# Kernel tuning notes

Hardware: AMD Instinct MI355X
Metric: run time of the kernel (lower is better)

The kernel has to match this reference:

```python
import jax, jax.numpy as jnp
import numpy as np

L = 3        # layer_num
D = 64       # hidden_size (input_dim)
NU = 100000  # user nodes in batched graph
NI = 100000  # item nodes in batched graph
NUSER = 200000  # user vocab
NITEM = 200000  # item vocab
E = 1000000  # edges per relation ('by' and 'pby')
B = 1024     # target users per batch


def _time_enc(t, freq, phase):
    # TimeEncode: cos(t * basis_freq + phase), per edge -> [E, D]
    return jnp.cos(t[:, None] * freq[None, :] + phase[None, :])


def _seg_attn(e, vals, dst, num_seg):
    # softmax of e over edges sharing a destination node, then weighted sum of vals
    m = jax.ops.segment_max(e, dst, num_segments=num_seg)
    ex = jnp.exp(e - m[dst])
    denom = jax.ops.segment_sum(ex, dst, num_segments=num_seg)
    alpha = ex / denom[dst]
    return jax.ops.segment_sum(alpha[:, None] * vals, dst, num_segments=num_seg)


def _forward(user_emb, item_emb, Wu, Wi, Wuu, Wii,
             u_freq, u_phase, uk_freq, uk_phase,
             i_freq, i_phase, ik_freq, ik_phase,
             unified_W, dense_W, dense_b,
             by_time, pby_time,
             user_id, item_id, by_src, by_dst, pby_src, pby_dst,
             user_index, last_item_index):
    nu = user_id.shape[0]
    ni = item_id.shape[0]
    d = user_emb.shape[1]
    scale = 1.0 / jnp.sqrt(jnp.float32(d))
    user_h = user_emb[user_id]   # [NU, D]
    item_h = item_emb[item_id]   # [NI, D]
    user_layers = []
    n_layers = Wu.shape[0]
    for l in range(n_layers):
        uh = user_h @ Wu[l]   # user_weight
        ih = item_h @ Wi[l]   # item_weight
        # --- 'by' relation: item -> user (user_reduce_func) ---
        src_i = ih[by_src]    # mailbox['item_h']
        dst_u = uh[by_dst]    # mailbox['user_h'] (dst feature)
        e_u = jnp.sum((_time_enc(by_time, u_freq[l], u_phase[l]) + src_i) * dst_u, -1) * scale
        agg_u = _seg_attn(e_u, src_i + _time_enc(by_time, uk_freq[l], uk_phase[l]), by_dst, nu)
        # --- 'pby' relation: user -> item (item_reduce_func) ---
        src_u = uh[pby_src]
        dst_i = ih[pby_dst]
        e_i = jnp.sum((_time_enc(pby_time, i_freq[l], i_phase[l]) + src_u) * dst_i, -1) * scale
        agg_i = _seg_attn(e_i, src_u + _time_enc(pby_time, ik_freq[l], ik_phase[l]), pby_dst, ni)
        # node update: elu(W [agg ; old])
        user_h = jax.nn.elu(jnp.concatenate([agg_u, user_h], -1) @ Wuu[l])
        item_h = jax.nn.elu(jnp.concatenate([agg_i, item_h], -1) @ Wii[l])
        user_layers.append(user_h[user_index])
    user_layers.append(item_h[last_item_index])  # last_item=True
    unified = jnp.concatenate(user_layers, -1) @ unified_W
    return jax.nn.relu(unified @ dense_W + dense_b)  # [B, 3]


def setup_inputs() -> dict:
    key = jax.random.key(0)
    ks = jax.random.split(key, 20)
    w = lambda k, shape: jax.random.normal(k, shape, jnp.float32) * 0.05
    freq0 = jnp.asarray(1.0 / 10 ** np.linspace(0, 9, D), dtype=jnp.float32)
    freq = jnp.tile(freq0[None], (L, 1))
    zph = jnp.zeros((L, D), jnp.float32)
    return {
        'user_emb': w(ks[0], (NUSER, D)),
        'item_emb': w(ks[1], (NITEM, D)),
        'Wu': w(ks[2], (L, D, D)),
        'Wi': w(ks[3], (L, D, D)),
        'Wuu': w(ks[4], (L, 2 * D, D)),
        'Wii': w(ks[5], (L, 2 * D, D)),
        'u_freq': freq, 'u_phase': zph,
        'uk_freq': freq, 'uk_phase': zph,
        'i_freq': freq, 'i_phase': zph,
        'ik_freq': freq, 'ik_phase': zph,
        'unified_W': w(ks[6], ((L + 1) * D, D)),
        'dense_W': w(ks[7], (D, 3)),
        'dense_b': jnp.zeros((3,), jnp.float32),
        'by_time': jax.random.uniform(ks[8], (E,), jnp.float32),
        'pby_time': jax.random.uniform(ks[9], (E,), jnp.float32),
        'user_id': jax.random.randint(ks[10], (NU,), 0, NUSER),
        'item_id': jax.random.randint(ks[11], (NI,), 0, NITEM),
        'by_src': jax.random.randint(ks[12], (E,), 0, NI),
        'by_dst': jax.random.randint(ks[13], (E,), 0, NU),
        'pby_src': jax.random.randint(ks[14], (E,), 0, NU),
        'pby_dst': jax.random.randint(ks[15], (E,), 0, NI),
        'user_index': jax.random.randint(ks[16], (B,), 0, NU),
        'last_item_index': jax.random.randint(ks[17], (B,), 0, NI),
    }


def reference(user_emb, item_emb, Wu, Wi, Wuu, Wii,
              u_freq, u_phase, uk_freq, uk_phase,
              i_freq, i_phase, ik_freq, ik_phase,
              unified_W, dense_W, dense_b,
              by_time, pby_time,
              user_id, item_id, by_src, by_dst, pby_src, pby_dst,
              user_index, last_item_index):
    return _forward(user_emb, item_emb, Wu, Wi, Wuu, Wii,
                    u_freq, u_phase, uk_freq, uk_phase,
                    i_freq, i_phase, ik_freq, ik_phase,
                    unified_W, dense_W, dense_b,
                    by_time, pby_time,
                    user_id, item_id, by_src, by_dst, pby_src, pby_dst,
                    user_index, last_item_index)
```

## Files before the change

kernel.cpp:

```cpp
#include <hip/hip_runtime.h>
#include <math.h>

#define D 64

typedef __attribute__((ext_vector_type(8))) short s8bf;
typedef __attribute__((ext_vector_type(4))) float fx4;

__device__ __forceinline__ float bf2f(unsigned short u) {
    union { unsigned int i; float f; } v; v.i = ((unsigned int)u) << 16; return v.f;
}
__device__ __forceinline__ unsigned short f2bf(float f) {
    union { float f; unsigned int i; } v; v.f = f;
    unsigned int r = v.i + 0x7FFFu + ((v.i >> 16) & 1u);
    return (unsigned short)(r >> 16);
}

__global__ __launch_bounds__(256) void k_gather2(const float* __restrict__ ue,
                                                 const float* __restrict__ ie,
                                                 const int* __restrict__ uid,
                                                 const int* __restrict__ iid,
                                                 float* __restrict__ uh0,
                                                 float* __restrict__ ih0, int NU, int NI) {
    int i = blockIdx.x * blockDim.x + threadIdx.x;
    if (i >= (NU + NI) * D) return;
    int r = i >> 6, c = i & 63;
    if (r < NU) uh0[(size_t)r * D + c] = ue[(size_t)uid[r] * D + c];
    else { int j = r - NU; ih0[(size_t)j * D + c] = ie[(size_t)iid[j] * D + c]; }
}

__global__ __launch_bounds__(256) void k_wprep(const float* __restrict__ Wu,
                                               const float* __restrict__ Wi,
                                               const float* __restrict__ Wuu,
                                               const float* __restrict__ Wii,
                                               unsigned short* __restrict__ WuT,
                                               unsigned short* __restrict__ WiT,
                                               unsigned short* __restrict__ WuuT,
                                               unsigned short* __restrict__ WiiT, int L) {
    int i = blockIdx.x * blockDim.x + threadIdx.x;
    int n1 = L * 64 * 64, n2 = L * 64 * 128;
    if (i < n1) {
        int l = i >> 12, c = (i >> 6) & 63, k = i & 63;
        WuT[i] = f2bf(Wu[l * 4096 + k * 64 + c]);
        WiT[i] = f2bf(Wi[l * 4096 + k * 64 + c]);
    }
    if (i < n2) {
        int l = i >> 13, c = (i >> 7) & 63, k = i & 127;
        WuuT[i] = f2bf(Wuu[l * 8192 + k * 64 + c]);
        WiiT[i] = f2bf(Wii[l * 8192 + k * 64 + c]);
    }
}

__global__ __launch_bounds__(256) void k_hist2(const int* __restrict__ bd,
                                               const int* __restrict__ pd,
                                               int* __restrict__ cu, int* __restrict__ ci, int E) {
    for (int i = blockIdx.x * blockDim.x + threadIdx.x; i < 2 * E; i += gridDim.x * blockDim.x) {
        if (i < E) atomicAdd(&cu[bd[i]], 1);
        else       atomicAdd(&ci[pd[i - E]], 1);
    }
}

__global__ __launch_bounds__(256) void k_scan_block2(const int* __restrict__ cu, int* __restrict__ rp_u,
                                                     const int* __restrict__ ci, int* __restrict__ rp_i,
                                                     int* __restrict__ bsums, int nbU, int NU, int NI) {
    __shared__ int ts[256];
    bool rel = blockIdx.x >= (unsigned)nbU;
    const int* in = rel ? ci : cu;
    int* out = rel ? rp_i : rp_u;
    int n = rel ? NI : NU;
    int boff = rel ? blockIdx.x - nbU : blockIdx.x;
    int t = threadIdx.x;
    int base = boff * 2048 + t * 8;
    int v[8]; int s = 0;
#pragma unroll
    for (int k = 0; k < 8; ++k) { int idx = base + k; v[k] = idx < n ? in[idx] : 0; s += v[k]; }
    ts[t] = s; __syncthreads();
    for (int off = 1; off < 256; off <<= 1) {
        int x = (t >= off) ? ts[t - off] : 0;
        __syncthreads(); ts[t] += x; __syncthreads();
    }
    int excl = ts[t] - s;
    if (t == 255) bsums[blockIdx.x] = ts[255];
    int run = excl;
#pragma unroll
    for (int k = 0; k < 8; ++k) { int idx = base + k; if (idx < n) out[idx] = run; run += v[k]; }
}

__global__ __launch_bounds__(256) void k_scan_small(int* __restrict__ bsums, int nbU, int nbI) {
    __shared__ int ts[256];
    int t = threadIdx.x;
    int half = t >> 7, local = t & 127;
    int nb = half ? nbI : nbU;
    int g = half ? nbU + local : local;
    int v = local < nb ? bsums[g] : 0;
    ts[t] = v; __syncthreads();
    for (int off = 1; off < 128; off <<= 1) {
        int x = (local >= off) ? ts[t - off] : 0;
        __syncthreads(); ts[t] += x; __syncthreads();
    }
    if (local < nb) bsums[g] = ts[t] - v;
}

__global__ __launch_bounds__(256) void k_fixup2(int* __restrict__ rp_u, int* __restrict__ rp_i,
                                                const int* __restrict__ bsums,
                                                int* __restrict__ cu, int* __restrict__ ci,
                                                int NU, int NI, int E, int nbU) {
    int i = blockIdx.x * blockDim.x + threadIdx.x;
    if (i < NU) {
        int v = rp_u[i] + bsums[i >> 11]; rp_u[i] = v; cu[i] = v;
        if (i == 0) rp_u[NU] = E;
    } else if (i < NU + NI) {
        int j = i - NU;
        int v = rp_i[j] + bsums[nbU + (j >> 11)]; rp_i[j] = v; ci[j] = v;
        if (j == 0) rp_i[NI] = E;
    }
}

__global__ __launch_bounds__(256) void k_scatter2(
    const int* __restrict__ bs, const int* __restrict__ bd, const float* __restrict__ bt,
    const int* __restrict__ ps, const int* __restrict__ pd, const float* __restrict__ pt,
    int* __restrict__ cu, int* __restrict__ ci,
    int2* __restrict__ bst, int* __restrict__ bdo_,
    int2* __restrict__ pst, int* __restrict__ pdo_, int E) {
    for (int i = blockIdx.x * blockDim.x + threadIdx.x; i < 2 * E; i += gridDim.x * blockDim.x) {
        if (i < E) {
            int d = bd[i]; int pos = atomicAdd(&cu[d], 1);
            bst[pos] = make_int2(bs[i], __float_as_int(bt[i])); bdo_[pos] = d;
        } else {
            int k = i - E;
            int d = pd[k]; int pos = atomicAdd(&ci[d], 1);
            pst[pos] = make_int2(ps[k], __float_as_int(pt[k])); pdo_[pos] = d;
        }
    }
}

__global__ __launch_bounds__(256) void k_transform4(
    const float* __restrict__ user_h, const float* __restrict__ item_h,
    const unsigned short* __restrict__ WuT_l, const unsigned short* __restrict__ WiT_l,
    unsigned short* __restrict__ uh, unsigned short* __restrict__ ih,
    int NU, int NI, int G) {
    bool rel = blockIdx.x >= (unsigned)G;
    int b = rel ? blockIdx.x - G : blockIdx.x;
    const float* in = rel ? item_h : user_h;
    const unsigned short* WT = rel ? WiT_l : WuT_l;
    unsigned short* out = rel ? ih : uh;
    int n = rel ? NI : NU;
    int lane = threadIdx.x & 63;
    int l15 = lane & 15, l4 = lane >> 4;
    s8bf bfr[8];
#pragma unroll
    for (int ct = 0; ct < 4; ++ct)
#pragma unroll
        for (int kk = 0; kk < 2; ++kk)
            bfr[ct * 2 + kk] = *(const s8bf*)&WT[(ct * 16 + l15) * 64 + kk * 32 + l4 * 8];
    int wave = b * 4 + (threadIdx.x >> 6);
    int nw = G * 4;
    int ntiles = (n + 15) >> 4;
    for (int t = wave; t < ntiles; t += nw) {
        int r = t * 16 + l15; if (r >= n) r = n - 1;
        s8bf afr[2];
#pragma unroll
        for (int kk = 0; kk < 2; ++kk) {
            const float4* ap = (const float4*)&in[(size_t)r * 64 + kk * 32 + l4 * 8];
            float4 x = ap[0], y = ap[1];
            s8bf f;
            f[0] = (short)f2bf(x.x); f[1] = (short)f2bf(x.y);
            f[2] = (short)f2bf(x.z); f[3] = (short)f2bf(x.w);
            f[4] = (short)f2bf(y.x); f[5] = (short)f2bf(y.y);
            f[6] = (short)f2bf(y.z); f[7] = (short)f2bf(y.w);
            afr[kk] = f;
        }
#pragma unroll
        for (int ct = 0; ct < 4; ++ct) {
            fx4 c = {0.f, 0.f, 0.f, 0.f};
            c = __builtin_amdgcn_mfma_f32_16x16x32_bf16(afr[0], bfr[ct * 2 + 0], c, 0, 0, 0);
            c = __builtin_amdgcn_mfma_f32_16x16x32_bf16(afr[1], bfr[ct * 2 + 1], c, 0, 0, 0);
#pragma unroll
            for (int i2 = 0; i2 < 4; ++i2) {
                int row = t * 16 + l4 * 4 + i2;
                if (row < n) out[(size_t)row * 64 + ct * 16 + l15] = f2bf(c[i2]);
            }
        }
    }
}

__global__ __launch_bounds__(256) void k_edge2(
    const unsigned short* __restrict__ ihF, const unsigned short* __restrict__ uhF,
    const int2* __restrict__ by_st, const int* __restrict__ by_d,
    const int2* __restrict__ pby_st, const int* __restrict__ pby_d,
    const float* __restrict__ uf, const float* __restrict__ up,
    const float* __restrict__ ukf, const float* __restrict__ ukp,
    const float* __restrict__ ifq, const float* __restrict__ ipq,
    const float* __restrict__ ikf, const float* __restrict__ ikp,
    float* __restrict__ agg_u, float* __restrict__ den_u,
    float* __restrict__ agg_i, float* __restrict__ den_i,
    int E, int EB) {
    bool rel = blockIdx.x >= (unsigned)EB;
    int rblk = rel ? blockIdx.x - EB : blockIdx.x;
    const unsigned short* srcF = rel ? uhF : ihF;
    const unsigned short* dstF = rel ? ihF : uhF;
    const int2* est = rel ? pby_st : by_st;
    const int* ed = rel ? pby_d : by_d;
    const float* efq = rel ? ifq : uf;
    const float* eps = rel ? ipq : up;
    const float* kfq = rel ? ikf : ukf;
    const float* kps = rel ? ikp : ukp;
    float* agg = rel ? agg_i : agg_u;
    float* den = rel ? den_i : den_u;

    int lane = threadIdx.x & 15;
    int grp  = threadIdx.x >> 4;
    int base = rblk * 256 + grp * 16;
    if (base >= E) return;
    float ef0 = efq[lane], ef1 = efq[lane + 16], ef2 = efq[lane + 32], ef3 = efq[lane + 48];
    float ep0 = eps[lane], ep1 = eps[lane + 16], ep2 = eps[lane + 32], ep3 = eps[lane + 48];
    float kf0 = kfq[lane], kf1 = kfq[lane + 16], kf2 = kfq[lane + 32], kf3 = kfq[lane + 48];
    float kp0 = kps[lane], kp1 = kps[lane + 16], kp2 = kps[lane + 32], kp3 = kps[lane + 48];
    bool same = ef0 == kf0 && ef1 == kf1 && ef2 == kf2 && ef3 == kf3 &&
                ep0 == kp0 && ep1 == kp1 && ep2 == kp2 && ep3 == kp3;
    same = __all(same);

    float a0 = 0, a1 = 0, a2 = 0, a3 = 0, dn = 0;
    float d0 = 0, d1 = 0, d2 = 0, d3 = 0;
    int cur = -1;
    for (int j = 0; j < 16; ++j) {
        int e = base + j;
        if (e >= E) break;
        int2 st = est[e];
        int s = st.x; float t = __int_as_float(st.y);
        int dd = ed[e];
        if (dd != cur) {
            if (cur >= 0) {
                float* ap = &agg[(size_t)cur * D + lane];
                unsafeAtomicAdd(ap +  0, a0); unsafeAtomicAdd(ap + 16, a1);
                unsafeAtomicAdd(ap + 32, a2); unsafeAtomicAdd(ap + 48, a3);
                if (lane == 0) unsafeAtomicAdd(&den[cur], dn);
            }
            a0 = a1 = a2 = a3 = 0; dn = 0; cur = dd;
            const unsigned short* dp = &dstF[(size_t)dd * D + lane];
            d0 = bf2f(dp[0]); d1 = bf2f(dp[16]); d2 = bf2f(dp[32]); d3 = bf2f(dp[48]);
        }
        const unsigned short* sp = &srcF[(size_t)s * D + lane];
        float s0 = bf2f(sp[0]), s1 = bf2f(sp[16]), s2 = bf2f(sp[32]), s3 = bf2f(sp[48]);
        float c0 = __cosf(fmaf(t, ef0, ep0));
        float c1 = __cosf(fmaf(t, ef1, ep1));
        float c2 = __cosf(fmaf(t, ef2, ep2));
        float c3 = __cosf(fmaf(t, ef3, ep3));
        float p = (c0 + s0) * d0 + (c1 + s1) * d1 + (c2 + s2) * d2 + (c3 + s3) * d3;
        p += __shfl_xor(p, 1); p += __shfl_xor(p, 2);
        p += __shfl_xor(p, 4); p += __shfl_xor(p, 8);
        float ex = __expf(p * 0.125f);
        float k0, k1, k2, k3;
        if (same) { k0 = c0; k1 = c1; k2 = c2; k3 = c3; }
        else {
            k0 = __cosf(fmaf(t, kf0, kp0)); k1 = __cosf(fmaf(t, kf1, kp1));
            k2 = __cosf(fmaf(t, kf2, kp2)); k3 = __cosf(fmaf(t, kf3, kp3));
        }
        a0 = fmaf(ex, s0 + k0, a0); a1 = fmaf(ex, s1 + k1, a1);
        a2 = fmaf(ex, s2 + k2, a2); a3 = fmaf(ex, s3 + k3, a3);
        dn += ex;
    }
    if (cur >= 0) {
        float* ap = &agg[(size_t)cur * D + lane];
        unsafeAtomicAdd(ap +  0, a0); unsafeAtomicAdd(ap + 16, a1);
        unsafeAtomicAdd(ap + 32, a2); unsafeAtomicAdd(ap + 48, a3);
        if (lane == 0) unsafeAtomicAdd(&den[cur], dn);
    }
}

__global__ __launch_bounds__(256) void k_update4(
    float* __restrict__ user_h, float* __restrict__ item_h,
    const float* __restrict__ agg_u, const float* __restrict__ den_u,
    const float* __restrict__ agg_i, const float* __restrict__ den_i,
    const unsigned short* __restrict__ WuuT_l, const unsigned short* __restrict__ WiiT_l,
    int NU, int NI, int G) {
    bool rel = blockIdx.x >= (unsigned)G;
    int b = rel ? blockIdx.x - G : blockIdx.x;
    float* h = rel ? item_h : user_h;
    const float* agg = rel ? agg_i : agg_u;
    const float* den = rel ? den_i : den_u;
    const unsigned short* WT = rel ? WiiT_l : WuuT_l;
    int n = rel ? NI : NU;
    int lane = threadIdx.x & 63;
    int l15 = lane & 15, l4 = lane >> 4;
    s8bf bfr[16];
#pragma unroll
    for (int ct = 0; ct < 4; ++ct)
#pragma unroll
        for (int kk = 0; kk < 4; ++kk)
            bfr[ct * 4 + kk] = *(const s8bf*)&WT[(ct * 16 + l15) * 128 + kk * 32 + l4 * 8];
    int wave = b * 4 + (threadIdx.x >> 6);
    int nw = G * 4;
    int ntiles = (n + 15) >> 4;
    for (int t = wave; t < ntiles; t += nw) {
        int r = t * 16 + l15; if (r >= n) r = n - 1;
        float dd = den[r];
        float inv = dd > 0.f ? 1.f / dd : 0.f;
        s8bf afr[4];
#pragma unroll
        for (int kk = 0; kk < 2; ++kk) {
            const float4* ap = (const float4*)&agg[(size_t)r * 64 + kk * 32 + l4 * 8];
            float4 x = ap[0], y = ap[1];
            s8bf f;
            f[0] = (short)f2bf(x.x * inv); f[1] = (short)f2bf(x.y * inv);
            f[2] = (short)f2bf(x.z * inv); f[3] = (short)f2bf(x.w * inv);
            f[4] = (short)f2bf(y.x * inv); f[5] = (short)f2bf(y.y * inv);
            f[6] = (short)f2bf(y.z * inv); f[7] = (short)f2bf(y.w * inv);
            afr[kk] = f;
        }
#pragma unroll
        for (int kk = 0; kk < 2; ++kk) {
            const float4* hp = (const float4*)&h[(size_t)r * 64 + kk * 32 + l4 * 8];
            float4 x = hp[0], y = hp[1];
            s8bf f;
            f[0] = (short)f2bf(x.x); f[1] = (short)f2bf(x.y);
            f[2] = (short)f2bf(x.z); f[3] = (short)f2bf(x.w);
            f[4] = (short)f2bf(y.x); f[5] = (short)f2bf(y.y);
            f[6] = (short)f2bf(y.z); f[7] = (short)f2bf(y.w);
            afr[2 + kk] = f;
        }
#pragma unroll
        for (int ct = 0; ct < 4; ++ct) {
            fx4 c = {0.f, 0.f, 0.f, 0.f};
            c = __builtin_amdgcn_mfma_f32_16x16x32_bf16(afr[0], bfr[ct * 4 + 0], c, 0, 0, 0);
            c = __builtin_amdgcn_mfma_f32_16x16x32_bf16(afr[1], bfr[ct * 4 + 1], c, 0, 0, 0);
            c = __builtin_amdgcn_mfma_f32_16x16x32_bf16(afr[2], bfr[ct * 4 + 2], c, 0, 0, 0);
            c = __builtin_amdgcn_mfma_f32_16x16x32_bf16(afr[3], bfr[ct * 4 + 3], c, 0, 0, 0);
#pragma unroll
            for (int i2 = 0; i2 < 4; ++i2) {
                int row = t * 16 + l4 * 4 + i2;
                if (row < n) {
                    float o = c[i2];
                    h[(size_t)row * 64 + ct * 16 + l15] = o > 0.f ? o : __expf(o) - 1.f;
                }
            }
        }
    }
}

__global__ __launch_bounds__(256) void k_gather_feat(const float* __restrict__ h,
                                                     const int* __restrict__ idx,
                                                     float* __restrict__ feat, int B,
                                                     int colOff, int FW) {
    int i = blockIdx.x * blockDim.x + threadIdx.x;
    if (i >= B * D) return;
    int b = i >> 6, c = i & 63;
    feat[(size_t)b * FW + colOff + c] = h[(size_t)idx[b] * D + c];
}

__global__ __launch_bounds__(64) void k_final(const float* __restrict__ feat,
                                              const float* __restrict__ uW,
                                              const float* __restrict__ dW,
                                              const float* __restrict__ db,
                                              float* __restrict__ out, int B, int FW) {
    __shared__ float fr[512];
    __shared__ float un[D];
    int b = blockIdx.x;
    int c = threadIdx.x;
    for (int i = c; i < FW; i += 64) fr[i] = feat[(size_t)b * FW + i];
    __syncthreads();
    float acc = 0.f;
    for (int d = 0; d < FW; ++d) acc += fr[d] * uW[d * D + c];
    un[c] = acc;
    __syncthreads();
    if (c < 3) {
        float o = db[c];
#pragma unroll
        for (int d = 0; d < D; ++d) o += un[d] * dW[d * 3 + c];
        out[b * 3 + c] = o > 0.f ? o : 0.f;
    }
}

extern "C" void kernel_launch(void* const* d_in, const int* in_sizes, int n_in,
                              void* d_out, int out_size, void* d_ws, size_t ws_size,
                              hipStream_t stream) {
    const float* user_emb = (const float*)d_in[0];
    const float* item_emb = (const float*)d_in[1];
    const float* Wu       = (const float*)d_in[2];
    const float* Wi       = (const float*)d_in[3];
    const float* Wuu      = (const float*)d_in[4];
    const float* Wii      = (const float*)d_in[5];
    const float* u_freq   = (const float*)d_in[6];
    const float* u_phase  = (const float*)d_in[7];
    const float* uk_freq  = (const float*)d_in[8];
    const float* uk_phase = (const float*)d_in[9];
    const float* i_freq   = (const float*)d_in[10];
    const float* i_phase  = (const float*)d_in[11];
    const float* ik_freq  = (const float*)d_in[12];
    const float* ik_phase = (const float*)d_in[13];
    const float* unified_W = (const float*)d_in[14];
    const float* dense_W   = (const float*)d_in[15];
    const float* dense_b   = (const float*)d_in[16];
    const float* by_time   = (const float*)d_in[17];
    const float* pby_time  = (const float*)d_in[18];
    const int* user_id   = (const int*)d_in[19];
    const int* item_id   = (const int*)d_in[20];
    const int* by_src    = (const int*)d_in[21];
    const int* by_dst    = (const int*)d_in[22];
    const int* pby_src   = (const int*)d_in[23];
    const int* pby_dst   = (const int*)d_in[24];
    const int* user_index = (const int*)d_in[25];
    const int* last_item_index = (const int*)d_in[26];

    const int NU = in_sizes[19];
    const int NI = in_sizes[20];
    const int E  = in_sizes[21];
    const int B  = in_sizes[25];
    const int L  = in_sizes[2] / (D * D);
    const int FW = (L + 1) * D;

    char* wp = (char*)d_ws;
    auto alloc_f = [&](size_t n) { float* p = (float*)wp; wp += n * sizeof(float); return p; };
    auto alloc_i = [&](size_t n) { int* p = (int*)wp; wp += n * sizeof(int); return p; };
    auto alloc_i2 = [&](size_t n) { int2* p = (int2*)wp; wp += n * sizeof(int2); return p; };
    auto alloc_h = [&](size_t n) { unsigned short* p = (unsigned short*)wp; wp += n * sizeof(unsigned short); return p; };
    float* agg_u = alloc_f((size_t)NU * D);
    float* agg_i = alloc_f((size_t)NI * D);
    float* den_u = alloc_f(NU);
    float* den_i = alloc_f(NI);
    size_t zero_bytes = (size_t)(wp - (char*)d_ws);
    int2* by_st  = alloc_i2(E);
    int2* pby_st = alloc_i2(E);
    int* cur_u = alloc_i(NU);
    int* cur_i = alloc_i(NI);
    size_t cur_bytes = (size_t)NU * 4 + (size_t)NI * 4;
    float* user_h = alloc_f((size_t)NU * D);
    float* item_h = alloc_f((size_t)NI * D);
    unsigned short* uh = alloc_h((size_t)NU * D);
    unsigned short* ih = alloc_h((size_t)NI * D);
    unsigned short* WuT  = alloc_h((size_t)L * 64 * 64);
    unsigned short* WiT  = alloc_h((size_t)L * 64 * 64);
    unsigned short* WuuT = alloc_h((size_t)L * 64 * 128);
    unsigned short* WiiT = alloc_h((size_t)L * 64 * 128);
    int*   by_dsts    = alloc_i(E);
    int*   pby_dsts   = alloc_i(E);
    int*   by_rowptr  = alloc_i(NU + 2);
    int*   pby_rowptr = alloc_i(NI + 2);
    int*   bsums      = alloc_i(512);
    float* feat       = alloc_f((size_t)B * FW);

    const int nbU = (NU + 2047) / 2048, nbI = (NI + 2047) / 2048;

    k_gather2<<<((NU + NI) * D + 255) / 256, 256, 0, stream>>>(
        user_emb, item_emb, user_id, item_id, user_h, item_h, NU, NI);
    k_wprep<<<(L * 64 * 128 + 255) / 256, 256, 0, stream>>>(Wu, Wi, Wuu, Wii,
                                                            WuT, WiT, WuuT, WiiT, L);

    hipMemsetAsync(cur_u, 0, cur_bytes, stream);
    k_hist2<<<2048, 256, 0, stream>>>(by_dst, pby_dst, cur_u, cur_i, E);
    k_scan_block2<<<nbU + nbI, 256, 0, stream>>>(cur_u, by_rowptr, cur_i, pby_rowptr,
                                                 bsums, nbU, NU, NI);
    k_scan_small<<<1, 256, 0, stream>>>(bsums, nbU, nbI);
    k_fixup2<<<(NU + NI + 255) / 256, 256, 0, stream>>>(by_rowptr, pby_rowptr, bsums,
                                                        cur_u, cur_i, NU, NI, E, nbU);
    k_scatter2<<<2048, 256, 0, stream>>>(by_src, by_dst, by_time,
                                         pby_src, pby_dst, pby_time,
                                         cur_u, cur_i,
                                         by_st, by_dsts,
                                         pby_st, pby_dsts, E);

    const int EB = (E + 255) / 256;
    const int GM = 512;
    for (int l = 0; l < L; ++l) {
        hipMemsetAsync(d_ws, 0, zero_bytes, stream);
        k_transform4<<<2 * GM, 256, 0, stream>>>(user_h, item_h,
                                                 WuT + (size_t)l * 4096, WiT + (size_t)l * 4096,
                                                 uh, ih, NU, NI, GM);
        k_edge2<<<2 * EB, 256, 0, stream>>>(
            ih, uh,
            by_st, by_dsts,
            pby_st, pby_dsts,
            u_freq + l * D, u_phase + l * D, uk_freq + l * D, uk_phase + l * D,
            i_freq + l * D, i_phase + l * D, ik_freq + l * D, ik_phase + l * D,
            agg_u, den_u, agg_i, den_i, E, EB);
        k_update4<<<2 * GM, 256, 0, stream>>>(user_h, item_h,
                                              agg_u, den_u, agg_i, den_i,
                                              WuuT + (size_t)l * 8192, WiiT + (size_t)l * 8192,
                                              NU, NI, GM);
        k_gather_feat<<<(B * D + 255) / 256, 256, 0, stream>>>(user_h, user_index, feat, B,
                                                               l * D, FW);
    }
    k_gather_feat<<<(B * D + 255) / 256, 256, 0, stream>>>(item_h, last_item_index, feat, B,
                                                           L * D, FW);
    k_final<<<B, 64, 0, stream>>>(feat, unified_W, dense_W, dense_b, (float*)d_out, B, FW);
}
```

Before: 732.9 us.

## Store node hidden states in bf16 and pack edge records into int4

The persistent user/item hidden states are now kept in bf16 instead of fp32, so transform and update load MFMA operand fragments directly and skip per-element conversion. This halves the bytes read and written for node features in every layer. The sorted edge arrays also merge source, time and destination into one int4 record, so each edge needs a single 16-byte load instead of two separate loads. In exchange, hidden states are rounded to bf16 between layers, which adds numerical error, and the padded edge record adds bytes to the scatter writes.

```diff
diff --git a/kernel.cpp b/kernel.cpp
--- a/kernel.cpp
+++ b/kernel.cpp
@@ -19,13 +19,13 @@
                                                  const float* __restrict__ ie,
                                                  const int* __restrict__ uid,
                                                  const int* __restrict__ iid,
-                                                 float* __restrict__ uh0,
-                                                 float* __restrict__ ih0, int NU, int NI) {
+                                                 unsigned short* __restrict__ uh0,
+                                                 unsigned short* __restrict__ ih0, int NU, int NI) {
     int i = blockIdx.x * blockDim.x + threadIdx.x;
     if (i >= (NU + NI) * D) return;
     int r = i >> 6, c = i & 63;
-    if (r < NU) uh0[(size_t)r * D + c] = ue[(size_t)uid[r] * D + c];
-    else { int j = r - NU; ih0[(size_t)j * D + c] = ie[(size_t)iid[j] * D + c]; }
+    if (r < NU) uh0[(size_t)r * D + c] = f2bf(ue[(size_t)uid[r] * D + c]);
+    else { int j = r - NU; ih0[(size_t)j * D + c] = f2bf(ie[(size_t)iid[j] * D + c]); }
 }
 
 __global__ __launch_bounds__(256) void k_wprep(const float* __restrict__ Wu,
@@ -119,28 +119,27 @@
     const int* __restrict__ bs, const int* __restrict__ bd, const float* __restrict__ bt,
     const int* __restrict__ ps, const int* __restrict__ pd, const float* __restrict__ pt,
     int* __restrict__ cu, int* __restrict__ ci,
-    int2* __restrict__ bst, int* __restrict__ bdo_,
-    int2* __restrict__ pst, int* __restrict__ pdo_, int E) {
+    int4* __restrict__ be, int4* __restrict__ pe, int E) {
     for (int i = blockIdx.x * blockDim.x + threadIdx.x; i < 2 * E; i += gridDim.x * blockDim.x) {
         if (i < E) {
             int d = bd[i]; int pos = atomicAdd(&cu[d], 1);
-            bst[pos] = make_int2(bs[i], __float_as_int(bt[i])); bdo_[pos] = d;
+            be[pos] = make_int4(bs[i], __float_as_int(bt[i]), d, 0);
         } else {
             int k = i - E;
             int d = pd[k]; int pos = atomicAdd(&ci[d], 1);
-            pst[pos] = make_int2(ps[k], __float_as_int(pt[k])); pdo_[pos] = d;
+            pe[pos] = make_int4(ps[k], __float_as_int(pt[k]), d, 0);
         }
     }
 }
 
 __global__ __launch_bounds__(256) void k_transform4(
-    const float* __restrict__ user_h, const float* __restrict__ item_h,
+    const unsigned short* __restrict__ user_h, const unsigned short* __restrict__ item_h,
     const unsigned short* __restrict__ WuT_l, const unsigned short* __restrict__ WiT_l,
     unsigned short* __restrict__ uh, unsigned short* __restrict__ ih,
     int NU, int NI, int G) {
     bool rel = blockIdx.x >= (unsigned)G;
     int b = rel ? blockIdx.x - G : blockIdx.x;
-    const float* in = rel ? item_h : user_h;
+    const unsigned short* in = rel ? item_h : user_h;
     const unsigned short* WT = rel ? WiT_l : WuT_l;
     unsigned short* out = rel ? ih : uh;
     int n = rel ? NI : NU;
@@ -157,23 +156,13 @@
     int ntiles = (n + 15) >> 4;
     for (int t = wave; t < ntiles; t += nw) {
         int r = t * 16 + l15; if (r >= n) r = n - 1;
-        s8bf afr[2];
-#pragma unroll
-        for (int kk = 0; kk < 2; ++kk) {
-            const float4* ap = (const float4*)&in[(size_t)r * 64 + kk * 32 + l4 * 8];
-            float4 x = ap[0], y = ap[1];
-            s8bf f;
-            f[0] = (short)f2bf(x.x); f[1] = (short)f2bf(x.y);
-            f[2] = (short)f2bf(x.z); f[3] = (short)f2bf(x.w);
-            f[4] = (short)f2bf(y.x); f[5] = (short)f2bf(y.y);
-            f[6] = (short)f2bf(y.z); f[7] = (short)f2bf(y.w);
-            afr[kk] = f;
-        }
+        s8bf afr0 = *(const s8bf*)&in[(size_t)r * 64 + l4 * 8];
+        s8bf afr1 = *(const s8bf*)&in[(size_t)r * 64 + 32 + l4 * 8];
 #pragma unroll
         for (int ct = 0; ct < 4; ++ct) {
             fx4 c = {0.f, 0.f, 0.f, 0.f};
-            c = __builtin_amdgcn_mfma_f32_16x16x32_bf16(afr[0], bfr[ct * 2 + 0], c, 0, 0, 0);
-            c = __builtin_amdgcn_mfma_f32_16x16x32_bf16(afr[1], bfr[ct * 2 + 1], c, 0, 0, 0);
+            c = __builtin_amdgcn_mfma_f32_16x16x32_bf16(afr0, bfr[ct * 2 + 0], c, 0, 0, 0);
+            c = __builtin_amdgcn_mfma_f32_16x16x32_bf16(afr1, bfr[ct * 2 + 1], c, 0, 0, 0);
 #pragma unroll
             for (int i2 = 0; i2 < 4; ++i2) {
                 int row = t * 16 + l4 * 4 + i2;
@@ -185,8 +174,7 @@
 
 __global__ __launch_bounds__(256) void k_edge2(
     const unsigned short* __restrict__ ihF, const unsigned short* __restrict__ uhF,
-    const int2* __restrict__ by_st, const int* __restrict__ by_d,
-    const int2* __restrict__ pby_st, const int* __restrict__ pby_d,
+    const int4* __restrict__ by_e, const int4* __restrict__ pby_e,
     const float* __restrict__ uf, const float* __restrict__ up,
     const float* __restrict__ ukf, const float* __restrict__ ukp,
     const float* __restrict__ ifq, const float* __restrict__ ipq,
@@ -198,8 +186,7 @@
     int rblk = rel ? blockIdx.x - EB : blockIdx.x;
     const unsigned short* srcF = rel ? uhF : ihF;
     const unsigned short* dstF = rel ? ihF : uhF;
-    const int2* est = rel ? pby_st : by_st;
-    const int* ed = rel ? pby_d : by_d;
+    const int4* ee = rel ? pby_e : by_e;
     const float* efq = rel ? ifq : uf;
     const float* eps = rel ? ipq : up;
     const float* kfq = rel ? ikf : ukf;
@@ -225,9 +212,8 @@
     for (int j = 0; j < 16; ++j) {
         int e = base + j;
         if (e >= E) break;
-        int2 st = est[e];
-        int s = st.x; float t = __int_as_float(st.y);
-        int dd = ed[e];
+        int4 q = ee[e];
+        int s = q.x; float t = __int_as_float(q.y); int dd = q.z;
         if (dd != cur) {
             if (cur >= 0) {
                 float* ap = &agg[(size_t)cur * D + lane];
@@ -268,14 +254,14 @@
 }
 
 __global__ __launch_bounds__(256) void k_update4(
-    float* __restrict__ user_h, float* __restrict__ item_h,
+    unsigned short* __restrict__ user_h, unsigned short* __restrict__ item_h,
     const float* __restrict__ agg_u, const float* __restrict__ den_u,
     const float* __restrict__ agg_i, const float* __restrict__ den_i,
     const unsigned short* __restrict__ WuuT_l, const unsigned short* __restrict__ WiiT_l,
     int NU, int NI, int G) {
     bool rel = blockIdx.x >= (unsigned)G;
     int b = rel ? blockIdx.x - G : blockIdx.x;
-    float* h = rel ? item_h : user_h;
+    unsigned short* h = rel ? item_h : user_h;
     const float* agg = rel ? agg_i : agg_u;
     const float* den = rel ? den_i : den_u;
     const unsigned short* WT = rel ? WiiT_l : WuuT_l;
@@ -307,17 +293,8 @@
             f[6] = (short)f2bf(y.z * inv); f[7] = (short)f2bf(y.w * inv);
             afr[kk] = f;
         }
-#pragma unroll
-        for (int kk = 0; kk < 2; ++kk) {
-            const float4* hp = (const float4*)&h[(size_t)r * 64 + kk * 32 + l4 * 8];
-            float4 x = hp[0], y = hp[1];
-            s8bf f;
-            f[0] = (short)f2bf(x.x); f[1] = (short)f2bf(x.y);
-            f[2] = (short)f2bf(x.z); f[3] = (short)f2bf(x.w);
-            f[4] = (short)f2bf(y.x); f[5] = (short)f2bf(y.y);
-            f[6] = (short)f2bf(y.z); f[7] = (short)f2bf(y.w);
-            afr[2 + kk] = f;
-        }
+        afr[2] = *(const s8bf*)&h[(size_t)r * 64 + l4 * 8];
+        afr[3] = *(const s8bf*)&h[(size_t)r * 64 + 32 + l4 * 8];
 #pragma unroll
         for (int ct = 0; ct < 4; ++ct) {
             fx4 c = {0.f, 0.f, 0.f, 0.f};
@@ -330,21 +307,22 @@
                 int row = t * 16 + l4 * 4 + i2;
                 if (row < n) {
                     float o = c[i2];
-                    h[(size_t)row * 64 + ct * 16 + l15] = o > 0.f ? o : __expf(o) - 1.f;
+                    h[(size_t)row * 64 + ct * 16 + l15] =
+                        f2bf(o > 0.f ? o : __expf(o) - 1.f);
                 }
             }
         }
     }
 }
 
-__global__ __launch_bounds__(256) void k_gather_feat(const float* __restrict__ h,
+__global__ __launch_bounds__(256) void k_gather_feat(const unsigned short* __restrict__ h,
                                                      const int* __restrict__ idx,
                                                      float* __restrict__ feat, int B,
                                                      int colOff, int FW) {
     int i = blockIdx.x * blockDim.x + threadIdx.x;
     if (i >= B * D) return;
     int b = i >> 6, c = i & 63;
-    feat[(size_t)b * FW + colOff + c] = h[(size_t)idx[b] * D + c];
+    feat[(size_t)b * FW + colOff + c] = bf2f(h[(size_t)idx[b] * D + c]);
 }
 
 __global__ __launch_bounds__(64) void k_final(const float* __restrict__ feat,
@@ -411,28 +389,26 @@
     char* wp = (char*)d_ws;
     auto alloc_f = [&](size_t n) { float* p = (float*)wp; wp += n * sizeof(float); return p; };
     auto alloc_i = [&](size_t n) { int* p = (int*)wp; wp += n * sizeof(int); return p; };
-    auto alloc_i2 = [&](size_t n) { int2* p = (int2*)wp; wp += n * sizeof(int2); return p; };
+    auto alloc_i4 = [&](size_t n) { int4* p = (int4*)wp; wp += n * sizeof(int4); return p; };
     auto alloc_h = [&](size_t n) { unsigned short* p = (unsigned short*)wp; wp += n * sizeof(unsigned short); return p; };
     float* agg_u = alloc_f((size_t)NU * D);
     float* agg_i = alloc_f((size_t)NI * D);
     float* den_u = alloc_f(NU);
     float* den_i = alloc_f(NI);
     size_t zero_bytes = (size_t)(wp - (char*)d_ws);
-    int2* by_st  = alloc_i2(E);
-    int2* pby_st = alloc_i2(E);
+    int4* by_e  = alloc_i4(E);
+    int4* pby_e = alloc_i4(E);
     int* cur_u = alloc_i(NU);
     int* cur_i = alloc_i(NI);
     size_t cur_bytes = (size_t)NU * 4 + (size_t)NI * 4;
-    float* user_h = alloc_f((size_t)NU * D);
-    float* item_h = alloc_f((size_t)NI * D);
+    unsigned short* user_h = alloc_h((size_t)NU * D);
+    unsigned short* item_h = alloc_h((size_t)NI * D);
     unsigned short* uh = alloc_h((size_t)NU * D);
     unsigned short* ih = alloc_h((size_t)NI * D);
     unsigned short* WuT  = alloc_h((size_t)L * 64 * 64);
     unsigned short* WiT  = alloc_h((size_t)L * 64 * 64);
     unsigned short* WuuT = alloc_h((size_t)L * 64 * 128);
     unsigned short* WiiT = alloc_h((size_t)L * 64 * 128);
-    int*   by_dsts    = alloc_i(E);
-    int*   pby_dsts   = alloc_i(E);
     int*   by_rowptr  = alloc_i(NU + 2);
     int*   pby_rowptr = alloc_i(NI + 2);
     int*   bsums      = alloc_i(512);
@@ -454,9 +430,7 @@
                                                         cur_u, cur_i, NU, NI, E, nbU);
     k_scatter2<<<2048, 256, 0, stream>>>(by_src, by_dst, by_time,
                                          pby_src, pby_dst, pby_time,
-                                         cur_u, cur_i,
-                                         by_st, by_dsts,
-                                         pby_st, pby_dsts, E);
+                                         cur_u, cur_i, by_e, pby_e, E);
 
     const int EB = (E + 255) / 256;
     const int GM = 512;
@@ -466,9 +440,7 @@
                                                  WuT + (size_t)l * 4096, WiT + (size_t)l * 4096,
                                                  uh, ih, NU, NI, GM);
         k_edge2<<<2 * EB, 256, 0, stream>>>(
-            ih, uh,
-            by_st, by_dsts,
-            pby_st, pby_dsts,
+            ih, uh, by_e, pby_e,
             u_freq + l * D, u_phase + l * D, uk_freq + l * D, uk_phase + l * D,
             i_freq + l * D, i_phase + l * D, ik_freq + l * D, ik_phase + l * D,
             agg_u, den_u, agg_i, den_i, E, EB);
```

Measured after the change: 740.2 us. No clear change (+1.0%).
